# Kernel tuning notes

Measured on AMD Instinct MI355X. Metric: run time of the kernel, lower is better.

## Reference

```python
import jax, jax.numpy as jnp
import numpy as np

N = 50000
E = 800000
IN_C, HID_C, LAT_C = 64, 64, 32


def setup_inputs() -> dict:
    key = jax.random.key(0)
    k = jax.random.split(key, 8)
    x = jax.random.normal(k[0], (N, IN_C), dtype=jnp.float32)
    edge_index = jax.random.randint(k[1], (2, E), 0, N, dtype=jnp.int64)
    edge_weight = jax.random.uniform(k[2], (E,), dtype=jnp.float32)
    # GCNConv parameters (glorot-style scale)
    W1 = jax.random.normal(k[3], (IN_C, HID_C), dtype=jnp.float32) * (1.0 / np.sqrt(IN_C))
    b1 = jnp.zeros((HID_C,), dtype=jnp.float32)
    W2 = jax.random.normal(k[4], (HID_C, LAT_C), dtype=jnp.float32) * (1.0 / np.sqrt(HID_C))
    b2 = jnp.zeros((LAT_C,), dtype=jnp.float32)
    return {"x": x, "edge_index": edge_index, "edge_weight": edge_weight,
            "W1": W1, "b1": b1, "W2": W2, "b2": b2}


def _gcn_norm(edge_index, edge_weight, num_nodes):
    # Add self loops (PyG GCNConv default: add_self_loops=True, fill_value=1.0)
    loop = jnp.arange(num_nodes, dtype=edge_index.dtype)
    src = jnp.concatenate([edge_index[0], loop])
    dst = jnp.concatenate([edge_index[1], loop])
    ew = jnp.concatenate([edge_weight, jnp.ones((num_nodes,), edge_weight.dtype)])
    # Symmetric normalization: deg computed at destination nodes
    deg = jax.ops.segment_sum(ew, dst, num_segments=num_nodes)
    dinv = jnp.where(deg > 0, jax.lax.rsqrt(deg), 0.0)
    norm = dinv[src] * ew * dinv[dst]  # [E + N]
    return src, dst, norm


def _gcn_conv(x, src, dst, norm, W, b, num_nodes):
    h = x @ W                                   # [N, out] dense transform first (out <= in)
    msg = h[src] * norm[:, None]                # gather + scale, [E+N, out]
    out = jax.ops.segment_sum(msg, dst, num_segments=num_nodes)  # scatter-add
    return out + b


def reference(x, edge_index, edge_weight, W1, b1, W2, b2):
    num_nodes = x.shape[0]
    src, dst, norm = _gcn_norm(edge_index, edge_weight, num_nodes)
    h = jax.nn.relu(_gcn_conv(x, src, dst, norm, W1, b1, num_nodes))
    z = jax.nn.relu(_gcn_conv(h, src, dst, norm, W2, b2, num_nodes))
    return z
```

## Files before the change

### kernel.cpp

```cpp
#include <hip/hip_runtime.h>
#include <hip/hip_fp16.h>

#define IN_C 64
#define HID_C 64
#define LAT_C 32
#define NMAX 50000
#define EMAX 800000
#define SLOTS 48
#define NB 196
#define CAP 5120
#define EPB 2048

__device__ float    g_dinv[NMAX];
__device__ __half   g_hf[NMAX * HID_C];
__device__ __half   g_gf[NMAX * LAT_C];
__device__ int      g_cnt[NMAX];
__device__ int      g_bcnt[NB];
__device__ uint2    g_bucket[(size_t)NB * CAP];
__device__ unsigned g_edgep[NMAX * SLOTS];


__global__ void k_zero_bcnt() {
    int i = threadIdx.x;
    if (i < NB) g_bcnt[i] = 0;
}

__global__ __launch_bounds__(256) void k_scatter1(const int* __restrict__ ei,
                                                  const float* __restrict__ ew, int E,
                                                  const float* __restrict__ x,
                                                  const float* __restrict__ W,
                                                  int n, int Bf) {
    __shared__ float sW[64 * 64];
    __shared__ float sX[4][4 * 72];
    __shared__ int hist[NB];
    __shared__ int base[NB];

    if ((int)blockIdx.x < Bf) {
        int t = threadIdx.x;
        for (int i = t; i < NB; i += 256) hist[i] = 0;
        __syncthreads();
        int e0 = blockIdx.x * EPB;
        int dv[8], sv[8], off[8];
        float wv[8];
#pragma unroll
        for (int i = 0; i < 8; ++i) {
            int e = e0 + t + i * 256;
            if (e < E) {
                dv[i] = ei[E + e];
                sv[i] = ei[e];
                wv[i] = ew[e];
                off[i] = atomicAdd(&hist[dv[i] >> 8], 1);
            } else dv[i] = -1;
        }
        __syncthreads();
        for (int i = t; i < NB; i += 256)
            base[i] = (hist[i] > 0) ? atomicAdd(&g_bcnt[i], hist[i]) : 0;
        __syncthreads();
#pragma unroll
        for (int i = 0; i < 8; ++i) {
            if (dv[i] >= 0) {
                int b = dv[i] >> 8;
                int pos = base[b] + off[i];
                if (pos < CAP) {
                    uint2 r;
                    r.x = ((unsigned)dv[i] << 16) | (unsigned)sv[i];
                    r.y = __float_as_uint(wv[i]);
                    g_bucket[(size_t)b * CAP + pos] = r;
                }
            }
        }
        return;
    }

    int bid = blockIdx.x - Bf;
    int t = threadIdx.x;
    int wave = t >> 6, lane = t & 63;
    int nodeBase = bid * 16 + wave * 4;

    {
        int w4 = lane * 4;
        int qq = w4 >> 6, kk = w4 & 63;
        int node = nodeBase + qq;
        float4 v = make_float4(0.f, 0.f, 0.f, 0.f);
        if (node < n) v = *(const float4*)&x[(size_t)node * 64 + kk];
        *(float4*)&sX[wave][qq * 72 + kk] = v;
    }
    for (int i = t * 4; i < 64 * 64; i += 256 * 4)
        *(float4*)&sW[i] = *(const float4*)&W[i];
    __syncthreads();

    int q = lane >> 4, r = lane & 15;
    float4 acc = make_float4(0.f, 0.f, 0.f, 0.f);
#pragma unroll
    for (int k4 = 0; k4 < 16; ++k4) {
        float4 xk = *(const float4*)&sX[wave][q * 72 + k4 * 4];
        float4 w0 = *(const float4*)&sW[(k4 * 4 + 0) * 64 + r * 4];
        float4 w1 = *(const float4*)&sW[(k4 * 4 + 1) * 64 + r * 4];
        float4 w2 = *(const float4*)&sW[(k4 * 4 + 2) * 64 + r * 4];
        float4 w3 = *(const float4*)&sW[(k4 * 4 + 3) * 64 + r * 4];
        acc.x += xk.x * w0.x; acc.y += xk.x * w0.y; acc.z += xk.x * w0.z; acc.w += xk.x * w0.w;
        acc.x += xk.y * w1.x; acc.y += xk.y * w1.y; acc.z += xk.y * w1.z; acc.w += xk.y * w1.w;
        acc.x += xk.z * w2.x; acc.y += xk.z * w2.y; acc.z += xk.z * w2.z; acc.w += xk.z * w2.w;
        acc.x += xk.w * w3.x; acc.y += xk.w * w3.y; acc.z += xk.w * w3.z; acc.w += xk.w * w3.w;
    }
    int node = nodeBase + q;
    if (node < n) {
        ushort4 hv;
        hv.x = __half_as_ushort(__float2half_rn(acc.x));
        hv.y = __half_as_ushort(__float2half_rn(acc.y));
        hv.z = __half_as_ushort(__float2half_rn(acc.z));
        hv.w = __half_as_ushort(__float2half_rn(acc.w));
        *(ushort4*)&g_hf[(size_t)node * 64 + r * 4] = hv;
    }
}

__global__ __launch_bounds__(256) void k_build2(int n) {
    __shared__ int   cntl[256];
    __shared__ float degl[256];
    __shared__ float dinvl[256];
    int t = threadIdx.x;
    cntl[t] = 0;
    degl[t] = 0.f;
    __syncthreads();
    int b = blockIdx.x;
    int m = min(g_bcnt[b], CAP);
    const uint2* buck = &g_bucket[(size_t)b * CAP];
    for (int i = t; i < m; i += 256) {
        uint2 r = buck[i];
        int d = r.x >> 16;
        int dloc = d & 255;
        float w = __uint_as_float(r.y);
        int slot = atomicAdd(&cntl[dloc], 1);
        atomicAdd(&degl[dloc], w);
        if (slot < SLOTS) {
            unsigned rec = ((r.x & 0xffffu) << 16) |
                           (unsigned)__half_as_ushort(__float2half_rn(w));
            g_edgep[(size_t)d * SLOTS + slot] = rec;
        }
    }
    __syncthreads();
    int d = (b << 8) + t;
    if (d < n) {
        int c = min(cntl[t], SLOTS);
        int cp = min((c + 3) & ~3, SLOTS);
        for (int s = c; s < cp; ++s) g_edgep[(size_t)d * SLOTS + s] = 0;
        g_cnt[d] = cp;
        float di = rsqrtf(1.0f + degl[t]);
        g_dinv[d] = di;
        dinvl[t] = di;
    }
    __syncthreads();
    int rowsBase = b << 8;
    for (int i = t; i < 256 * 32; i += 256) {
        int r = i >> 5, el = i & 31;
        int d2 = rowsBase + r;
        if (d2 < n) {
            __half2* p = (__half2*)&g_hf[(size_t)d2 * 64] + el;
            float2 v = __half22float2(*p);
            float sc = dinvl[r];
            *p = __floats2half2_rn(v.x * sc, v.y * sc);
        }
    }
}

__global__ __launch_bounds__(256) void k_gather_fuse(const float* __restrict__ b1,
                                                     const float* __restrict__ W2, int n) {
    __shared__ float sW[64 * 32];
    __shared__ float sB[64];
    __shared__ float sA[32][68];
    int t = threadIdx.x;
    for (int i = t * 4; i < 64 * 32; i += 256 * 4)
        *(float4*)&sW[i] = *(const float4*)&W2[i];
    if (t < 64) sB[t] = b1[t];

    int lane = t & 63;
    int g = lane >> 3;
    int o = lane & 7;
    int nl = (t >> 6) * 8 + g;
    int w = blockIdx.x * 32 + nl;

    int len = (w < n) ? g_cnt[w] : 0;
    float dd = (w < n) ? g_dinv[w] : 0.f;
    unsigned o16 = (unsigned)(o * 16);
    const char* hb = (const char*)g_hf;

    float4 s0a = make_float4(0.f, 0.f, 0.f, 0.f), s0b = s0a;
    float4 s1a = s0a, s1b = s0a, s2a = s0a, s2b = s0a, s3a = s0a, s3b = s0a;
    if (w < n) {
        uint4 rr = *(const uint4*)(hb + ((unsigned)w << 7) + o16);
        float2 f0 = __half22float2(*(__half2*)&rr.x);
        float2 f1 = __half22float2(*(__half2*)&rr.y);
        float2 f2 = __half22float2(*(__half2*)&rr.z);
        float2 f3 = __half22float2(*(__half2*)&rr.w);
        s0a = make_float4(f0.x, f0.y, f1.x, f1.y);
        s0b = make_float4(f2.x, f2.y, f3.x, f3.y);
    }
    const unsigned* row = &g_edgep[(size_t)w * SLOTS];
#define GSTEP8(AL, AH, E) { \
    float nn = __half2float(__ushort_as_half((unsigned short)((E) & 0xffffu))); \
    unsigned off = (((E) >> 9) & 0xFFFFFF80u) | o16; \
    uint4 rr = *(const uint4*)(hb + off); \
    float2 f0 = __half22float2(*(__half2*)&rr.x); \
    float2 f1 = __half22float2(*(__half2*)&rr.y); \
    float2 f2 = __half22float2(*(__half2*)&rr.z); \
    float2 f3 = __half22float2(*(__half2*)&rr.w); \
    AL.x += f0.x * nn; AL.y += f0.y * nn; AL.z += f1.x * nn; AL.w += f1.y * nn; \
    AH.x += f2.x * nn; AH.y += f2.y * nn; AH.z += f3.x * nn; AH.w += f3.y * nn; }
    for (int j = 0; j < len; j += 4) {
        uint4 ra = *(const uint4*)&row[j];
        GSTEP8(s0a, s0b, ra.x) GSTEP8(s1a, s1b, ra.y)
        GSTEP8(s2a, s2b, ra.z) GSTEP8(s3a, s3b, ra.w)
    }
#undef GSTEP8
    float4 avl, avh;
    avl.x = ((s0a.x + s1a.x) + (s2a.x + s3a.x)) * dd;
    avl.y = ((s0a.y + s1a.y) + (s2a.y + s3a.y)) * dd;
    avl.z = ((s0a.z + s1a.z) + (s2a.z + s3a.z)) * dd;
    avl.w = ((s0a.w + s1a.w) + (s2a.w + s3a.w)) * dd;
    avh.x = ((s0b.x + s1b.x) + (s2b.x + s3b.x)) * dd;
    avh.y = ((s0b.y + s1b.y) + (s2b.y + s3b.y)) * dd;
    avh.z = ((s0b.z + s1b.z) + (s2b.z + s3b.z)) * dd;
    avh.w = ((s0b.w + s1b.w) + (s2b.w + s3b.w)) * dd;
    *(float4*)&sA[nl][8 * o] = avl;
    *(float4*)&sA[nl][8 * o + 4] = avh;
    __syncthreads();

    int nl2 = t >> 3;
    int c4 = (t & 7) * 4;
    int w2 = blockIdx.x * 32 + nl2;
    float4 gacc = make_float4(0.f, 0.f, 0.f, 0.f);
#pragma unroll
    for (int k = 0; k < 64; ++k) {
        float ak = fmaxf(sA[nl2][k] + sB[k], 0.f);
        float4 wk = *(const float4*)&sW[k * 32 + c4];
        gacc.x += ak * wk.x; gacc.y += ak * wk.y;
        gacc.z += ak * wk.z; gacc.w += ak * wk.w;
    }
    if (w2 < n) {
        float dd2 = g_dinv[w2];
        __half2 h0 = __floats2half2_rn(gacc.x * dd2, gacc.y * dd2);
        __half2 h1 = __floats2half2_rn(gacc.z * dd2, gacc.w * dd2);
        uint2 pk; pk.x = *(unsigned*)&h0; pk.y = *(unsigned*)&h1;
        *(uint2*)&g_gf[(size_t)w2 * 32 + c4] = pk;
    }
}

__global__ __launch_bounds__(256) void k_gather32(float* __restrict__ out,
                                                  const float* __restrict__ b2, int n) {
    int t = threadIdx.x;
    int lane = t & 63;
    int g = lane >> 3;
    int v = lane & 7;
    int hw = blockIdx.x * 32 + (t >> 6) * 8 + g;
    if (hw >= n) return;
    int len = g_cnt[hw];
    float dd = g_dinv[hw];
    unsigned v8 = (unsigned)(v * 8);
    const char* gb = (const char*)g_gf;

    float4 a0, a1 = make_float4(0.f, 0.f, 0.f, 0.f), a2 = a1, a3 = a1;
    {
        uint2 rr = *(const uint2*)(gb + ((unsigned)hw << 6) + v8);
        float2 f0 = __half22float2(*(__half2*)&rr.x);
        float2 f1 = __half22float2(*(__half2*)&rr.y);
        a0 = make_float4(f0.x, f0.y, f1.x, f1.y);
    }
    const unsigned* row = &g_edgep[(size_t)hw * SLOTS];
#define GSTEP32Q(ACC, E) { \
    float nn = __half2float(__ushort_as_half((unsigned short)((E) & 0xffffu))); \
    unsigned off = (((E) >> 10) & 0xFFFFFFC0u) | v8; \
    uint2 rr = *(const uint2*)(gb + off); \
    float2 f0 = __half22float2(*(__half2*)&rr.x); \
    float2 f1 = __half22float2(*(__half2*)&rr.y); \
    ACC.x += f0.x * nn; ACC.y += f0.y * nn; ACC.z += f1.x * nn; ACC.w += f1.y * nn; }
    for (int j = 0; j < len; j += 4) {
        uint4 ra = *(const uint4*)&row[j];
        GSTEP32Q(a0, ra.x) GSTEP32Q(a1, ra.y) GSTEP32Q(a2, ra.z) GSTEP32Q(a3, ra.w)
    }
#undef GSTEP32Q
    float4 bb = *(const float4*)&b2[4 * v];
    float4 o4;
    o4.x = fmaxf(((a0.x + a1.x) + (a2.x + a3.x)) * dd + bb.x, 0.f);
    o4.y = fmaxf(((a0.y + a1.y) + (a2.y + a3.y)) * dd + bb.y, 0.f);
    o4.z = fmaxf(((a0.z + a1.z) + (a2.z + a3.z)) * dd + bb.z, 0.f);
    o4.w = fmaxf(((a0.w + a1.w) + (a2.w + a3.w)) * dd + bb.w, 0.f);
    *(float4*)&out[(size_t)hw * 32 + 4 * v] = o4;
}


extern "C" void kernel_launch(void* const* d_in, const int* in_sizes, int n_in,
                              void* d_out, int out_size, void* d_ws, size_t ws_size,
                              hipStream_t stream) {
    const float* x  = (const float*)d_in[0];
    const int*   ei = (const int*)d_in[1];
    const float* ew = (const float*)d_in[2];
    const float* W1 = (const float*)d_in[3];
    const float* b1 = (const float*)d_in[4];
    const float* W2 = (const float*)d_in[5];
    const float* b2 = (const float*)d_in[6];
    float* out = (float*)d_out;

    int n = in_sizes[0] / IN_C;
    if (n > NMAX) n = NMAX;
    int E = in_sizes[2];
    if (E > EMAX) E = EMAX;

    int Bf = (E + EPB - 1) / EPB;
    int Bg = (n + 15) / 16;

    k_zero_bcnt<<<1, 256, 0, stream>>>();

    k_scatter1<<<Bf + Bg, 256, 0, stream>>>(ei, ew, E, x, W1, n, Bf);

    k_build2<<<NB, 256, 0, stream>>>(n);

    k_gather_fuse<<<(n + 31) / 32, 256, 0, stream>>>(b1, W2, n);

    k_gather32<<<(n + 31) / 32, 256, 0, stream>>>(out, b2, n);
}
```

Measured before the change: 93.44 us.

## Bin destination nodes by degree and process gathers in degree-sorted order

Destination nodes are grouped into bins by padded edge count during the build step. A scan kernel and a permutation kernel then build a degree-sorted node order, and both gather kernels use it. The aim is to cut warp divergence and load imbalance from uneven row lengths within a wavefront. In exchange it adds two extra kernel launches, an indirection load per node, and less locality for the self-row reads and output writes.

```diff
diff --git a/kernel.cpp b/kernel.cpp
--- a/kernel.cpp
+++ b/kernel.cpp
@@ -10,6 +10,7 @@
 #define NB 196
 #define CAP 5120
 #define EPB 2048
+#define NBIN 13
 
 __device__ float    g_dinv[NMAX];
 __device__ __half   g_hf[NMAX * HID_C];
@@ -18,11 +19,16 @@
 __device__ int      g_bcnt[NB];
 __device__ uint2    g_bucket[(size_t)NB * CAP];
 __device__ unsigned g_edgep[NMAX * SLOTS];
+__device__ int      g_bincnt[NBIN];
+__device__ int      g_binbase[NBIN];
+__device__ int      g_binbuf[NBIN * NMAX];
+__device__ int      g_perm[NMAX];
 
 
 __global__ void k_zero_bcnt() {
     int i = threadIdx.x;
     if (i < NB) g_bcnt[i] = 0;
+    if (i < NBIN) g_bincnt[i] = 0;
 }
 
 __global__ __launch_bounds__(256) void k_scatter1(const int* __restrict__ ei,
@@ -118,9 +124,12 @@
     __shared__ int   cntl[256];
     __shared__ float degl[256];
     __shared__ float dinvl[256];
+    __shared__ int   binh[NBIN];
+    __shared__ int   binb[NBIN];
     int t = threadIdx.x;
     cntl[t] = 0;
     degl[t] = 0.f;
+    if (t < NBIN) binh[t] = 0;
     __syncthreads();
     int b = blockIdx.x;
     int m = min(g_bcnt[b], CAP);
@@ -140,6 +149,7 @@
     }
     __syncthreads();
     int d = (b << 8) + t;
+    int bin = -1, boff = 0;
     if (d < n) {
         int c = min(cntl[t], SLOTS);
         int cp = min((c + 3) & ~3, SLOTS);
@@ -148,7 +158,14 @@
         float di = rsqrtf(1.0f + degl[t]);
         g_dinv[d] = di;
         dinvl[t] = di;
-    }
+        bin = cp >> 2;
+        boff = atomicAdd(&binh[bin], 1);
+    }
+    __syncthreads();
+    if (t < NBIN) binb[t] = (binh[t] > 0) ? atomicAdd(&g_bincnt[t], binh[t]) : 0;
+    __syncthreads();
+    if (bin >= 0)
+        g_binbuf[bin * NMAX + binb[bin] + boff] = d;
     __syncthreads();
     int rowsBase = b << 8;
     for (int i = t; i < 256 * 32; i += 256) {
@@ -163,6 +180,20 @@
     }
 }
 
+__global__ void k_binscan() {
+    if (threadIdx.x == 0) {
+        int acc = 0;
+        for (int i = 0; i < NBIN; ++i) { g_binbase[i] = acc; acc += g_bincnt[i]; }
+    }
+}
+
+__global__ void k_perm() {
+    int i = blockIdx.x * blockDim.x + threadIdx.x;
+    int bin = i / NMAX, j = i - bin * NMAX;
+    if (bin < NBIN && j < g_bincnt[bin])
+        g_perm[g_binbase[bin] + j] = g_binbuf[i];
+}
+
 __global__ __launch_bounds__(256) void k_gather_fuse(const float* __restrict__ b1,
                                                      const float* __restrict__ W2, int n) {
     __shared__ float sW[64 * 32];
@@ -177,16 +208,17 @@
     int g = lane >> 3;
     int o = lane & 7;
     int nl = (t >> 6) * 8 + g;
-    int w = blockIdx.x * 32 + nl;
-
-    int len = (w < n) ? g_cnt[w] : 0;
-    float dd = (w < n) ? g_dinv[w] : 0.f;
+    int slot = blockIdx.x * 32 + nl;
+    int w = (slot < n) ? g_perm[slot] : -1;
+
+    int len = (w >= 0) ? g_cnt[w] : 0;
+    float dd = (w >= 0) ? g_dinv[w] : 0.f;
     unsigned o16 = (unsigned)(o * 16);
     const char* hb = (const char*)g_hf;
 
     float4 s0a = make_float4(0.f, 0.f, 0.f, 0.f), s0b = s0a;
     float4 s1a = s0a, s1b = s0a, s2a = s0a, s2b = s0a, s3a = s0a, s3b = s0a;
-    if (w < n) {
+    if (w >= 0) {
         uint4 rr = *(const uint4*)(hb + ((unsigned)w << 7) + o16);
         float2 f0 = __half22float2(*(__half2*)&rr.x);
         float2 f1 = __half22float2(*(__half2*)&rr.y);
@@ -195,7 +227,7 @@
         s0a = make_float4(f0.x, f0.y, f1.x, f1.y);
         s0b = make_float4(f2.x, f2.y, f3.x, f3.y);
     }
-    const unsigned* row = &g_edgep[(size_t)w * SLOTS];
+    const unsigned* row = (w >= 0) ? &g_edgep[(size_t)w * SLOTS] : g_edgep;
 #define GSTEP8(AL, AH, E) { \
     float nn = __half2float(__ushort_as_half((unsigned short)((E) & 0xffffu))); \
     unsigned off = (((E) >> 9) & 0xFFFFFF80u) | o16; \
@@ -227,7 +259,7 @@
 
     int nl2 = t >> 3;
     int c4 = (t & 7) * 4;
-    int w2 = blockIdx.x * 32 + nl2;
+    int slot2 = blockIdx.x * 32 + nl2;
     float4 gacc = make_float4(0.f, 0.f, 0.f, 0.f);
 #pragma unroll
     for (int k = 0; k < 64; ++k) {
@@ -236,7 +268,8 @@
         gacc.x += ak * wk.x; gacc.y += ak * wk.y;
         gacc.z += ak * wk.z; gacc.w += ak * wk.w;
     }
-    if (w2 < n) {
+    if (slot2 < n) {
+        int w2 = g_perm[slot2];
         float dd2 = g_dinv[w2];
         __half2 h0 = __floats2half2_rn(gacc.x * dd2, gacc.y * dd2);
         __half2 h1 = __floats2half2_rn(gacc.z * dd2, gacc.w * dd2);
@@ -251,8 +284,9 @@
     int lane = t & 63;
     int g = lane >> 3;
     int v = lane & 7;
-    int hw = blockIdx.x * 32 + (t >> 6) * 8 + g;
-    if (hw >= n) return;
+    int slot = blockIdx.x * 32 + (t >> 6) * 8 + g;
+    if (slot >= n) return;
+    int hw = g_perm[slot];
     int len = g_cnt[hw];
     float dd = g_dinv[hw];
     unsigned v8 = (unsigned)(v * 8);
@@ -314,6 +348,9 @@
 
     k_build2<<<NB, 256, 0, stream>>>(n);
 
+    k_binscan<<<1, 64, 0, stream>>>();
+    k_perm<<<(NBIN * NMAX + 255) / 256, 256, 0, stream>>>();
+
     k_gather_fuse<<<(n + 31) / 32, 256, 0, stream>>>(b1, W2, n);
 
     k_gather32<<<(n + 31) / 32, 256, 0, stream>>>(out, b2, n);
```

Result: slower. 97.22 us (+4.0%).
